# Kernel optimization log

Measured on AMD Instinct MI355X. Metric: run time of the kernel, lower is better.

The kernel has to match this reference:

```python
import jax, jax.numpy as jnp
import numpy as np

HEADS = 8

def setup_inputs() -> dict:
    key = jax.random.key(0)
    ks = jax.random.split(key, 5)
    B, S, C = 2, 4096, 640
    s = 1.0 / np.sqrt(C)
    return {
        "hidden_states": jax.random.normal(ks[0], (B, S, C), dtype=jnp.float32),
        "Wq": jax.random.normal(ks[1], (C, C), dtype=jnp.float32) * s,
        "bq": jnp.zeros((C,), dtype=jnp.float32),
        "Wk": jax.random.normal(ks[2], (C, C), dtype=jnp.float32) * s,
        "bk": jnp.zeros((C,), dtype=jnp.float32),
        "Wv": jax.random.normal(ks[3], (C, C), dtype=jnp.float32) * s,
        "bv": jnp.zeros((C,), dtype=jnp.float32),
        "Wo": jax.random.normal(ks[4], (C, C), dtype=jnp.float32) * s,
        "bo": jnp.zeros((C,), dtype=jnp.float32),
    }


def reference(hidden_states, Wq, bq, Wk, bk, Wv, bv, Wo, bo):
    # Self-attention (encoder_hidden_states=None), no mask, no norms.
    B, S, C = hidden_states.shape
    H = HEADS
    D = C // H  # head_dim
    residual = hidden_states

    q = hidden_states @ Wq + bq  # [B,S,C]
    k = hidden_states @ Wk + bk
    v = hidden_states @ Wv + bv

    # [B,S,C] -> [B,H,S,D]
    q = q.reshape(B, S, H, D).transpose(0, 2, 1, 3)
    k = k.reshape(B, S, H, D).transpose(0, 2, 1, 3)
    v = v.reshape(B, S, H, D).transpose(0, 2, 1, 3)

    scale = 1.0 / np.sqrt(D)
    scores = jnp.einsum('bhqd,bhkd->bhqk', q, k) * scale  # [B,H,S,S]
    probs = jax.nn.softmax(scores, axis=-1)               # materialized, as in source
    out = jnp.einsum('bhqk,bhkd->bhqd', probs, v)         # [B,H,S,D]

    out = out.transpose(0, 2, 1, 3).reshape(B, S, C)
    out = out @ Wo + bo  # to_out[0]; to_out[1] is dropout (identity in eval)
    out = out + residual  # residual_connection=True
    return out            # rescale_output_factor = 1.0
```

## Files before the change

kernel.cpp:

```cpp
#include <hip/hip_runtime.h>
#include <hip/hip_bf16.h>
#include <stdint.h>

typedef __attribute__((ext_vector_type(8))) short short8;
typedef __attribute__((ext_vector_type(4))) short short4v;
typedef __attribute__((ext_vector_type(4))) float f32x4;
typedef __attribute__((ext_vector_type(16))) float f32x16;
typedef unsigned short u16;
typedef unsigned int u32;

#define DEV __device__ __forceinline__

constexpr int Bb = 2, Ss = 4096, Cc = 640, Hh = 8, Dd = 80;
constexpr int BS = Bb * Ss;
constexpr int NQKV = 3 * Cc;
constexpr int QKst = 2 * Cc;

DEV float bf2f(u16 u) { unsigned v = ((unsigned)u) << 16; float f; __builtin_memcpy(&f, &v, 4); return f; }
DEV u16 f2bf(float f) {
    unsigned u; __builtin_memcpy(&u, &f, 4);
    u += 0x7fffu + ((u >> 16) & 1u);
    return (u16)(u >> 16);
}
DEV u32 packbf2(float a, float b) {
    float2 f2; f2.x = a; f2.y = b;
    __hip_bfloat162 h2 = __float22bfloat162_rn(f2);
    u32 r; __builtin_memcpy(&r, &h2, 4);
    return r;
}

DEV void pswapf(float &a, float &b) {
#if __has_builtin(__builtin_amdgcn_permlane32_swap)
    auto r = __builtin_amdgcn_permlane32_swap(__float_as_int(a), __float_as_int(b), false, false);
    a = __int_as_float(r[0]); b = __int_as_float(r[1]);
#else
    float sa = __shfl_xor(a, 32, 64), sb = __shfl_xor(b, 32, 64);
    bool hi = (threadIdx.x & 32) != 0;
    float na = hi ? sb : a, nb = hi ? b : sa;
    a = na; b = nb;
#endif
}

#define GLD16(gp, lp) __builtin_amdgcn_global_load_lds( \
    (const __attribute__((address_space(1))) void*)(gp), \
    (__attribute__((address_space(3))) void*)(lp), 16, 0, 0)

__global__ __launch_bounds__(256) void prep_kernel(
    const float* __restrict__ hs,
    const float* __restrict__ Wq, const float* __restrict__ Wk,
    const float* __restrict__ Wv, const float* __restrict__ Wo,
    const float* __restrict__ bq, const float* __restrict__ bk,
    const float* __restrict__ bv,
    u16* __restrict__ Xb, float* __restrict__ bcat,
    u16* __restrict__ WTqkv, u16* __restrict__ WTo)
{
    const float QS = 0.11180339887498949f * 1.4426950408889634f;
    if (blockIdx.x < 1600) {
        __shared__ float T[32][33];
        int tile = blockIdx.x;
        int wsel = tile / 400;
        int tt = tile - wsel * 400;
        int tr = tt / 20, tc = tt - (tt / 20) * 20;
        const float* W = (wsel == 0) ? Wq : (wsel == 1) ? Wk : (wsel == 2) ? Wv : Wo;
        float sc = (wsel == 0) ? QS : 1.0f;
        int r = threadIdx.x >> 3, c4 = (threadIdx.x & 7) * 4;
        float4 v = *(const float4*)(W + (size_t)(tr * 32 + r) * Cc + tc * 32 + c4);
        T[r][c4 + 0] = v.x; T[r][c4 + 1] = v.y; T[r][c4 + 2] = v.z; T[r][c4 + 3] = v.w;
        __syncthreads();
        short4v o;
#pragma unroll
        for (int j = 0; j < 4; j++) o[j] = (short)f2bf(T[c4 + j][r] * sc);
        u16* dst = (wsel < 3) ? (WTqkv + (size_t)(wsel * Cc + tc * 32 + r) * Cc + tr * 32 + c4)
                              : (WTo + (size_t)(tc * 32 + r) * Cc + tr * 32 + c4);
        *(short4v*)dst = o;
    } else {
        int tid = (blockIdx.x - 1600) * blockDim.x + threadIdx.x;
        int nthr = 2048 * blockDim.x;
        for (int i = tid; i < BS * Cc / 4; i += nthr) {
            float4 v = ((const float4*)hs)[i];
            short4v o;
            o[0] = (short)f2bf(v.x); o[1] = (short)f2bf(v.y);
            o[2] = (short)f2bf(v.z); o[3] = (short)f2bf(v.w);
            ((short4v*)Xb)[i] = o;
        }
        for (int i = tid; i < NQKV; i += nthr) {
            float v = (i < Cc) ? bq[i] * QS : (i < 2 * Cc) ? bk[i - Cc] : bv[i - 2 * Cc];
            bcat[i] = v;
        }
    }
}

__global__ __launch_bounds__(256) void gemm_qkv(
    const u16* __restrict__ A, const u16* __restrict__ Bt,
    const float* __restrict__ bias, u16* __restrict__ QK,
    u16* __restrict__ VTg)
{
    __shared__ __align__(16) char gsm[32768];

    const int mBase = blockIdx.x * 128;
    const int nBase = blockIdx.y * 128;
    const int t = threadIdx.x, lane = t & 63, w = t >> 6;
    const int wr = w >> 1, wc = w & 1;
    const int l15 = lane & 15, g = lane >> 4;

    const int r0 = t >> 2, r1 = (t + 256) >> 2;
    const int cg0 = (t & 3) ^ (r0 & 3);
    const int cg1 = (t & 3) ^ (r1 & 3);
    const u16* pa0 = A + (size_t)(mBase + r0) * Cc + cg0 * 8;
    const u16* pa1 = A + (size_t)(mBase + r1) * Cc + cg1 * 8;
    const u16* pb0 = Bt + (size_t)(nBase + r0) * Cc + cg0 * 8;
    const u16* pb1 = Bt + (size_t)(nBase + r1) * Cc + cg1 * 8;

    auto stage = [&](int k0, int buf) {
        GLD16(pa0 + k0, gsm + buf * 8192 + w * 1024);
        GLD16(pa1 + k0, gsm + buf * 8192 + 4096 + w * 1024);
        GLD16(pb0 + k0, gsm + 16384 + buf * 8192 + w * 1024);
        GLD16(pb1 + k0, gsm + 16384 + buf * 8192 + 4096 + w * 1024);
    };

    stage(0, 0);
    __syncthreads();

    f32x4 acc[4][4] = {};
    const int lof = l15 * 64 + ((g ^ (l15 & 3)) << 4);
    int cur = 0;

    for (int k0 = 0; k0 < Cc; k0 += 32) {
        if (k0 + 32 < Cc) stage(k0 + 32, cur ^ 1);
        short8 af[4], bf[4];
#pragma unroll
        for (int i = 0; i < 4; i++) {
            af[i] = *(const short8*)(gsm + cur * 8192 + wr * 4096 + i * 1024 + lof);
            bf[i] = *(const short8*)(gsm + 16384 + cur * 8192 + wc * 4096 + i * 1024 + lof);
        }
#pragma unroll
        for (int mi = 0; mi < 4; mi++)
#pragma unroll
            for (int ni = 0; ni < 4; ni++)
                acc[mi][ni] = __builtin_amdgcn_mfma_f32_16x16x32_bf16(af[mi], bf[ni], acc[mi][ni], 0, 0, 0);
        __syncthreads();
        cur ^= 1;
    }

    if (nBase < 2 * Cc) {
#pragma unroll
        for (int mi = 0; mi < 4; mi++)
#pragma unroll
            for (int ni = 0; ni < 4; ni++) {
                int col = nBase + wc * 64 + ni * 16 + l15;
                float bb = bias[col];
#pragma unroll
                for (int r = 0; r < 4; r++) {
                    int row = mBase + wr * 64 + mi * 16 + g * 4 + r;
                    QK[(size_t)row * QKst + col] = f2bf(acc[mi][ni][r] + bb);
                }
            }
    } else {
        const int gp = ((g & 1) << 1) | (g >> 1);
#pragma unroll
        for (int mi = 0; mi < 4; mi++)
#pragma unroll
            for (int ni = 0; ni < 4; ni++) {
                int colg = nBase + wc * 64 + ni * 16 + l15;
                float bb = bias[colg];
                int vc = colg - 2 * Cc;
                int h = vc / Dd, d = vc - h * Dd;
                int row0 = mBase + wr * 64 + mi * 16 + gp * 4;
                int b = (mBase >> 12), s = row0 & 4095;
                short4v o;
#pragma unroll
                for (int r = 0; r < 4; r++) o[r] = (short)f2bf(acc[mi][ni][r] + bb);
                *(short4v*)(VTg + ((size_t)(b * Hh + h) * Dd + d) * Ss + s) = o;
            }
    }
}

constexpr int OBP = 88;

__global__ __launch_bounds__(256, 4) void attn_kernel(
    const u16* __restrict__ QK, const u16* __restrict__ VTg,
    u16* __restrict__ N0, u16* __restrict__ N1, u16* __restrict__ N2,
    float* __restrict__ Mp, float* __restrict__ Lp, int ns)
{
    __shared__ __align__(16) char smem[22528];

    const int id = blockIdx.x;
    const int per_qt = 16 * ns;
    const int qt = id / per_qt;
    const int rest = id - qt * per_qt;
    const int bh = rest / ns;
    const int si = rest - bh * ns;
    const int b = bh >> 3, h = bh & 7;
    const int t = threadIdx.x, lane = t & 63, w = t >> 6;
    const int l31 = lane & 31, e = lane >> 5;

    const size_t rowBase = (size_t)b * Ss;
    const int q0 = qt * 128;
    const int startT = (ns == 2) ? si * 32 : (si == 0 ? 0 : (si == 1 ? 22 : 43));
    const int NT = (ns == 2) ? 32 : (si == 0 ? 22 : 21);
    const int kvBase = startT * 64;

    const int lq8 = lane >> 3;
    const int vcg = (lane & 7) ^ lq8;
    const u16* kg0 = QK + (rowBase + kvBase + lane) * QKst + Cc + h * Dd;
    const u16* vg0 = VTg + ((size_t)bh * Dd) * Ss + kvBase + vcg * 8;

    for (int i = t; i < 512; i += 256)
        ((u32*)(smem + 20480))[i] = 0x3F803F80u;

    short8 qB[5];
    {
        const u16* qp = QK + (rowBase + q0 + w * 32 + l31) * QKst + h * Dd + e * 8;
#pragma unroll
        for (int ks = 0; ks < 5; ks++) qB[ks] = *(const short8*)(qp + ks * 16);
    }

    auto stageK = [&](int kt) {
#pragma unroll
        for (int j = 0; j < 3; j++) {
            int gi = w + 4 * j;
            if (gi < 10)
                GLD16(kg0 + (size_t)kt * 64 * QKst + gi * 8, smem + gi * 1024);
        }
    };
    auto stageV = [&](int kt) {
#pragma unroll
        for (int j = 0; j < 3; j++) {
            int gi = w + 4 * j;
            if (gi < 10)
                GLD16(vg0 + (size_t)(gi * 8 + lq8) * Ss + kt * 64,
                      smem + 10240 + gi * 1024);
        }
    };

    stageK(0);
    stageV(0);
    __syncthreads();

    float mrow = -1e30f;
    f32x16 oacc[3] = {};
    const int csl_base = l31 & 7;

    for (int kt = 0; kt < NT; ++kt) {
        const bool more = (kt + 1 < NT);

        f32x16 s2[2];
        __builtin_amdgcn_s_setprio(1);
#pragma unroll
        for (int n = 0; n < 2; n++) {
            f32x16 a = {};
#pragma unroll
            for (int ks = 0; ks < 5; ks++) {
                short8 kf = *(const short8*)(smem + ((2 * ks + e) * 64 + n * 32 + l31) * 16);
                a = __builtin_amdgcn_mfma_f32_32x32x16_bf16(kf, qB[ks], a, 0, 0, 0);
            }
            s2[n] = a;
        }
        __builtin_amdgcn_s_setprio(0);

        __syncthreads();
        if (more) stageK(kt + 1);

#define SV(j) ((j) < 16 ? s2[0][(j)] : s2[1][(j) - 16])
        float tt[11];
#pragma unroll
        for (int i = 0; i < 10; i++)
            tt[i] = fmaxf(fmaxf(SV(3 * i), SV(3 * i + 1)), SV(3 * i + 2));
        tt[10] = fmaxf(SV(30), SV(31));
#undef SV
        float u0 = fmaxf(fmaxf(tt[0], tt[1]), tt[2]);
        float u1 = fmaxf(fmaxf(tt[3], tt[4]), tt[5]);
        float u2 = fmaxf(fmaxf(tt[6], tt[7]), tt[8]);
        float u3 = fmaxf(tt[9], tt[10]);
        float vm = fmaxf(fmaxf(u0, u1), fmaxf(u2, u3));
        { float va = vm, vb = vm; pswapf(va, vb); vm = fmaxf(va, vb); }

        if (__any(vm > mrow + 8.0f)) {
            float mnew = fmaxf(mrow, vm);
            float al = __builtin_amdgcn_exp2f(mrow - mnew);
            mrow = mnew;
#pragma unroll
            for (int n = 0; n < 3; n++)
#pragma unroll
                for (int r = 0; r < 16; r++) oacc[n][r] *= al;
        }

        u32 pd[2][8];
#pragma unroll
        for (int n = 0; n < 2; n++)
#pragma unroll
            for (int m = 0; m < 8; m++) {
                float pa = __builtin_amdgcn_exp2f(s2[n][2 * m] - mrow);
                float pb = __builtin_amdgcn_exp2f(s2[n][2 * m + 1] - mrow);
                pd[n][m] = packbf2(pa, pb);
            }

        __builtin_amdgcn_s_setprio(1);
#pragma unroll
        for (int ks = 0; ks < 4; ks++) {
            const int n = ks >> 1, bb2 = ks & 1;
            union { u32 u[4]; short8 v; } pB;
            pB.u[0] = pd[n][4 * bb2 + 0];
            pB.u[1] = pd[n][4 * bb2 + 1];
            pB.u[2] = pd[n][4 * bb2 + 2];
            pB.u[3] = pd[n][4 * bb2 + 3];
            const int csl = (2 * ks + e) ^ csl_base;
#pragma unroll
            for (int n2 = 0; n2 < 3; n2++) {
                short8 vf = *(const short8*)(smem + 10240 + ((n2 * 32 + l31) * 8 + csl) * 16);
                oacc[n2] = __builtin_amdgcn_mfma_f32_32x32x16_bf16(vf, pB.v, oacc[n2], 0, 0, 0);
            }
        }
        __builtin_amdgcn_s_setprio(0);

        __syncthreads();
        if (more) stageV(kt + 1);
    }

    if (e == 0) {
        int mi = si * 65536 + bh * Ss + q0 + w * 32 + l31;
        Mp[mi] = mrow;
        Lp[mi] = oacc[2][8];
    }

    u16* Ob = (u16*)smem;
#pragma unroll
    for (int n = 0; n < 3; n++)
#pragma unroll
        for (int r = 0; r < 16; r += 2) {
            if (n == 2 && r >= 8) continue;
            int dloc = n * 32 + (r & 3) + 8 * (r >> 2) + 4 * e;
            u32 pk = packbf2(oacc[n][r], oacc[n][r + 1]);
            *(u32*)&Ob[(w * 32 + l31) * OBP + dloc] = pk;
        }
    __syncthreads();

    u16* Np = (si == 0) ? N0 : ((si == 1) ? N1 : N2);
    const int cb = h * Dd;
#pragma unroll
    for (int i = 0; i < 5; i++) {
        int gidx = i * 256 + t;
        int row = gidx / 10, gi = gidx % 10;
        short8 v = *(const short8*)&Ob[row * OBP + gi * 8];
        *(short8*)(Np + (rowBase + q0 + row) * Cc + cb + gi * 8) = v;
    }
}

__global__ __launch_bounds__(256) void gemm_oproj(
    const u16* __restrict__ N0, const u16* __restrict__ N1,
    const u16* __restrict__ N2, const u16* __restrict__ Bt,
    const float* __restrict__ Mp, const float* __restrict__ Lp,
    const float* __restrict__ bias, const float* __restrict__ resid,
    float* __restrict__ Out, int ns)
{
    __shared__ __align__(16) char osm[30720];
    float* WF = (float*)(osm + 24576);

    const int mBase = blockIdx.x * 64;
    const int nBase = blockIdx.y * 128;
    const int t = threadIdx.x, lane = t & 63, w = t >> 6;
    const int wr = w >> 1, wc = w & 1;
    const int l15 = lane & 15, g = lane >> 4;

    for (int i = t; i < 512; i += 256) {
        int r = i >> 3, h = i & 7;
        int row = mBase + r;
        int bb = row >> 12, q = row & 4095;
        int mi = (bb * 8 + h) * Ss + q;
        float m0 = Mp[mi], m1 = Mp[65536 + mi];
        float m2 = (ns == 3) ? Mp[131072 + mi] : -1e30f;
        float l0 = Lp[mi], l1 = Lp[65536 + mi];
        float l2 = (ns == 3) ? Lp[131072 + mi] : 1.0f;
        float m = fmaxf(fmaxf(m0, m1), m2);
        float w0 = exp2f(m0 - m), w1 = exp2f(m1 - m), w2 = exp2f(m2 - m);
        float rl = 1.0f / (l0 * w0 + l1 * w1 + l2 * w2);
        WF[(r * 8 + h) * 3 + 0] = w0 * rl;
        WF[(r * 8 + h) * 3 + 1] = w1 * rl;
        WF[(r * 8 + h) * 3 + 2] = w2 * rl;
    }

    const int rA = t >> 2, clA = t & 3;
    const int cgA = clA ^ (rA & 3);
    const int rB0 = t >> 2, rB1 = (t + 256) >> 2;
    const int cgB0 = (t & 3) ^ (rB0 & 3);
    const int cgB1 = (t & 3) ^ (rB1 & 3);
    const u16* pA0 = N0 + (size_t)(mBase + rA) * Cc + cgA * 8;
    const u16* pA1 = N1 + (size_t)(mBase + rA) * Cc + cgA * 8;
    const u16* pA2 = N2 + (size_t)(mBase + rA) * Cc + cgA * 8;
    const u16* pB0 = Bt + (size_t)(nBase + rB0) * Cc + cgB0 * 8;
    const u16* pB1 = Bt + (size_t)(nBase + rB1) * Cc + cgB1 * 8;

    auto stageB = [&](int k0, int buf) {
        GLD16(pB0 + k0, osm + 8192 + buf * 8192 + w * 1024);
        GLD16(pB1 + k0, osm + 8192 + buf * 8192 + 4096 + w * 1024);
    };
    auto stageA = [&](int k0, int buf) {
        int kA = k0 + cgA * 8;
        int hA = kA / 80;
        float w0 = WF[(rA * 8 + hA) * 3], w1 = WF[(rA * 8 + hA) * 3 + 1],
              w2 = WF[(rA * 8 + hA) * 3 + 2];
        short8 a0 = *(const short8*)(pA0 + k0);
        short8 c0 = *(const short8*)(pA1 + k0);
        short8 d0 = *(const short8*)(pA2 + k0);
        union { u32 u[4]; short8 v; } mg;
#pragma unroll
        for (int j = 0; j < 4; j++)
            mg.u[j] = packbf2(
                bf2f((u16)a0[2 * j]) * w0 + bf2f((u16)c0[2 * j]) * w1 + bf2f((u16)d0[2 * j]) * w2,
                bf2f((u16)a0[2 * j + 1]) * w0 + bf2f((u16)c0[2 * j + 1]) * w1 + bf2f((u16)d0[2 * j + 1]) * w2);
        *(short8*)(osm + buf * 4096 + rA * 64 + clA * 16) = mg.v;
    };

    __syncthreads();
    stageB(0, 0);
    stageA(0, 0);
    __syncthreads();

    f32x4 acc[2][4] = {};
    const int lof = l15 * 64 + ((g ^ (l15 & 3)) << 4);
    int cur = 0;

    for (int k0 = 0; k0 < Cc; k0 += 32) {
        const bool more = (k0 + 32 < Cc);
        if (more) stageB(k0 + 32, cur ^ 1);
        short8 af[2], bf[4];
#pragma unroll
        for (int i = 0; i < 2; i++)
            af[i] = *(const short8*)(osm + cur * 4096 + wr * 2048 + i * 1024 + lof);
#pragma unroll
        for (int i = 0; i < 4; i++)
            bf[i] = *(const short8*)(osm + 8192 + cur * 8192 + wc * 4096 + i * 1024 + lof);
#pragma unroll
        for (int mi = 0; mi < 2; mi++)
#pragma unroll
            for (int ni = 0; ni < 4; ni++)
                acc[mi][ni] = __builtin_amdgcn_mfma_f32_16x16x32_bf16(af[mi], bf[ni], acc[mi][ni], 0, 0, 0);
        if (more) stageA(k0 + 32, cur ^ 1);
        __syncthreads();
        cur ^= 1;
    }

#pragma unroll
    for (int mi = 0; mi < 2; mi++)
#pragma unroll
        for (int ni = 0; ni < 4; ni++) {
            int col = nBase + wc * 64 + ni * 16 + l15;
            float bb = bias[col];
#pragma unroll
            for (int r = 0; r < 4; r++) {
                int row = mBase + wr * 32 + mi * 16 + g * 4 + r;
                Out[(size_t)row * Cc + col] = acc[mi][ni][r] + bb + resid[(size_t)row * Cc + col];
            }
        }
}

extern "C" void kernel_launch(void* const* d_in, const int* in_sizes, int n_in,
                              void* d_out, int out_size, void* d_ws, size_t ws_size,
                              hipStream_t stream) {
    (void)in_sizes; (void)n_in; (void)out_size;
    const float* hs = (const float*)d_in[0];
    const float* Wq = (const float*)d_in[1];
    const float* bq = (const float*)d_in[2];
    const float* Wk = (const float*)d_in[3];
    const float* bk = (const float*)d_in[4];
    const float* Wv = (const float*)d_in[5];
    const float* bv = (const float*)d_in[6];
    const float* Wo = (const float*)d_in[7];
    const float* bo = (const float*)d_in[8];
    float* out = (float*)d_out;

    char* ws = (char*)d_ws;
    u16*   Xb    = (u16*)  (ws + 0);
    u16*   WTqkv = (u16*)  (ws + 10485760);
    u16*   WTo   = (u16*)  (ws + 12943360);
    float* bcat  = (float*)(ws + 13762560);
    u16*   QK    = (u16*)  (ws + 13770240);
    u16*   VTg   = (u16*)  (ws + 34741760);
    u16*   AOb   = (u16*)  (ws + 45227520);
    float* Mp    = (float*)(ws + 55713280);
    float* Lp    = (float*)(ws + 56499712);
    u16*   N2b   = (u16*)  (ws + 57286144);
    u16*   N1    = Xb;

    const int ns = (ws_size >= 67771904ULL) ? 3 : 2;
    u16* N2 = (ns == 3) ? N2b : AOb;

    prep_kernel<<<dim3(3648), dim3(256), 0, stream>>>(hs, Wq, Wk, Wv, Wo, bq, bk, bv,
                                                      Xb, bcat, WTqkv, WTo);
    gemm_qkv<<<dim3(64, 15), dim3(256), 0, stream>>>(Xb, WTqkv, bcat, QK, VTg);
    attn_kernel<<<dim3(32 * 16 * ns), dim3(256), 0, stream>>>(QK, VTg, AOb, N1, N2, Mp, Lp, ns);
    gemm_oproj<<<dim3(128, 5), dim3(256), 0, stream>>>(AOb, N1, N2, WTo, Mp, Lp, bo, hs, out, ns);
}
```

Baseline: 185.2 us.

## Double-buffer K/V tiles in LDS with one barrier per iteration

The attention loop now keeps two LDS buffers, each holding a K tile and a V tile, and loads them together two tiles ahead of use. The two per-iteration barriers and the split K/V staging are replaced by a single barrier followed by a combined prefetch into the buffer just consumed. The aim is to hide global-to-LDS latency and cut synchronisation. In exchange, LDS per block doubles to about 44 KB, which may reduce how many blocks fit on each CU. If the barrier drains all outstanding loads, the extra prefetch depth may also bring little benefit.

```diff
diff --git a/kernel.cpp b/kernel.cpp
--- a/kernel.cpp
+++ b/kernel.cpp
@@ -182,7 +182,7 @@
     u16* __restrict__ N0, u16* __restrict__ N1, u16* __restrict__ N2,
     float* __restrict__ Mp, float* __restrict__ Lp, int ns)
 {
-    __shared__ __align__(16) char smem[22528];
+    __shared__ __align__(16) char smem[45056];
 
     const int id = blockIdx.x;
     const int per_qt = 16 * ns;
@@ -205,8 +205,10 @@
     const u16* kg0 = QK + (rowBase + kvBase + lane) * QKst + Cc + h * Dd;
     const u16* vg0 = VTg + ((size_t)bh * Dd) * Ss + kvBase + vcg * 8;
 
-    for (int i = t; i < 512; i += 256)
+    for (int i = t; i < 512; i += 256) {
         ((u32*)(smem + 20480))[i] = 0x3F803F80u;
+        ((u32*)(smem + 22528 + 20480))[i] = 0x3F803F80u;
+    }
 
     short8 qB[5];
     {
@@ -215,26 +217,23 @@
         for (int ks = 0; ks < 5; ks++) qB[ks] = *(const short8*)(qp + ks * 16);
     }
 
-    auto stageK = [&](int kt) {
-#pragma unroll
-        for (int j = 0; j < 3; j++) {
+    auto stage = [&](int kt, int buf) {
+        char* base = smem + buf * 22528;
+#pragma unroll
+        for (int j = 0; j < 5; j++) {
             int gi = w + 4 * j;
-            if (gi < 10)
-                GLD16(kg0 + (size_t)kt * 64 * QKst + gi * 8, smem + gi * 1024);
+            if (gi < 10) {
+                GLD16(kg0 + (size_t)kt * 64 * QKst + gi * 8, base + gi * 1024);
+            } else {
+                int c = gi - 10;
+                GLD16(vg0 + (size_t)(c * 8 + lq8) * Ss + kt * 64,
+                      base + 10240 + c * 1024);
+            }
         }
     };
-    auto stageV = [&](int kt) {
-#pragma unroll
-        for (int j = 0; j < 3; j++) {
-            int gi = w + 4 * j;
-            if (gi < 10)
-                GLD16(vg0 + (size_t)(gi * 8 + lq8) * Ss + kt * 64,
-                      smem + 10240 + gi * 1024);
-        }
-    };
-
-    stageK(0);
-    stageV(0);
+
+    stage(0, 0);
+    stage(1, 1);
     __syncthreads();
 
     float mrow = -1e30f;
@@ -242,7 +241,8 @@
     const int csl_base = l31 & 7;
 
     for (int kt = 0; kt < NT; ++kt) {
-        const bool more = (kt + 1 < NT);
+        const char* kb = smem + (kt & 1) * 22528;
+        const char* vb = kb + 10240;
 
         f32x16 s2[2];
         __builtin_amdgcn_s_setprio(1);
@@ -251,15 +251,12 @@
             f32x16 a = {};
 #pragma unroll
             for (int ks = 0; ks < 5; ks++) {
-                short8 kf = *(const short8*)(smem + ((2 * ks + e) * 64 + n * 32 + l31) * 16);
+                short8 kf = *(const short8*)(kb + ((2 * ks + e) * 64 + n * 32 + l31) * 16);
                 a = __builtin_amdgcn_mfma_f32_32x32x16_bf16(kf, qB[ks], a, 0, 0, 0);
             }
             s2[n] = a;
         }
         __builtin_amdgcn_s_setprio(0);
-
-        __syncthreads();
-        if (more) stageK(kt + 1);
 
 #define SV(j) ((j) < 16 ? s2[0][(j)] : s2[1][(j) - 16])
         float tt[11];
@@ -273,7 +270,7 @@
         float u2 = fmaxf(fmaxf(tt[6], tt[7]), tt[8]);
         float u3 = fmaxf(tt[9], tt[10]);
         float vm = fmaxf(fmaxf(u0, u1), fmaxf(u2, u3));
-        { float va = vm, vb = vm; pswapf(va, vb); vm = fmaxf(va, vb); }
+        { float va = vm, vb2 = vm; pswapf(va, vb2); vm = fmaxf(va, vb2); }
 
         if (__any(vm > mrow + 8.0f)) {
             float mnew = fmaxf(mrow, vm);
@@ -307,14 +304,14 @@
             const int csl = (2 * ks + e) ^ csl_base;
 #pragma unroll
             for (int n2 = 0; n2 < 3; n2++) {
-                short8 vf = *(const short8*)(smem + 10240 + ((n2 * 32 + l31) * 8 + csl) * 16);
+                short8 vf = *(const short8*)(vb + ((n2 * 32 + l31) * 8 + csl) * 16);
                 oacc[n2] = __builtin_amdgcn_mfma_f32_32x32x16_bf16(vf, pB.v, oacc[n2], 0, 0, 0);
             }
         }
         __builtin_amdgcn_s_setprio(0);
 
         __syncthreads();
-        if (more) stageV(kt + 1);
+        if (kt + 2 < NT) stage(kt + 2, kt & 1);
     }
 
     if (e == 0) {
```

Result: no change. 188.8 us (+2.0%).
